# Kernel tuning notes

Measured on AMD Instinct MI355X. Metric: run time of the kernel, lower is better.

The kernel has to match this reference:

```python
import jax, jax.numpy as jnp
import numpy as np

D_IN = 1024
D_OUT = 1024
NUM_HEADS = 16
HEAD_DIM = D_OUT // NUM_HEADS


def setup_inputs() -> dict:
    key = jax.random.key(0)
    ks = jax.random.split(key, 6)
    scale = 0.02
    x = jax.random.normal(ks[0], (8, 1024, D_IN), dtype=jnp.float32)
    # weights stored as [in, out] (transposed vs torch Linear.weight)
    W_query = jax.random.normal(ks[1], (D_IN, D_OUT), dtype=jnp.float32) * scale
    W_key = jax.random.normal(ks[2], (D_IN, HEAD_DIM), dtype=jnp.float32) * scale
    W_value = jax.random.normal(ks[3], (D_IN, HEAD_DIM), dtype=jnp.float32) * scale
    W_out = jax.random.normal(ks[4], (D_OUT, D_OUT), dtype=jnp.float32) * scale
    b_out = jax.random.normal(ks[5], (D_OUT,), dtype=jnp.float32) * scale
    return {"x": x, "W_query": W_query, "W_key": W_key, "W_value": W_value,
            "W_out": W_out, "b_out": b_out}


def reference(x, W_query, W_key, W_value, W_out, b_out):
    B, S, _ = x.shape
    H, Dh = NUM_HEADS, HEAD_DIM
    q = (x @ W_query).reshape(B, S, H, Dh).transpose(0, 2, 1, 3)  # [B,H,S,Dh]
    k = x @ W_key      # [B,S,Dh] single shared head
    v = x @ W_value    # [B,S,Dh]
    # scores: broadcast shared K across all query heads (no explicit repeat)
    scores = jnp.einsum("bhqd,bkd->bhqk", q, k)  # [B,H,S,S]
    causal = jnp.triu(jnp.ones((S, S), dtype=bool), k=1)
    scores = jnp.where(causal[None, None], -jnp.inf, scores)
    attn = jax.nn.softmax(scores / np.sqrt(Dh).astype(np.float32), axis=-1)
    # dropout p=0.0 -> identity
    ctx = jnp.einsum("bhqk,bkd->bhqd", attn, v)  # [B,H,S,Dh]
    ctx = ctx.transpose(0, 2, 1, 3).reshape(B, S, H * Dh)
    return ctx @ W_out + b_out
```

## Files before the change

kernel.cpp:

```cpp
#include <hip/hip_runtime.h>

typedef unsigned short u16;
typedef __attribute__((ext_vector_type(8))) short short8;
typedef __attribute__((ext_vector_type(4))) float f32x4;
typedef __attribute__((ext_vector_type(16))) float f32x16;
typedef __attribute__((ext_vector_type(4))) unsigned short u16x4;
typedef __attribute__((ext_vector_type(4))) int i32x4;

__device__ __forceinline__ u16 f2b(float f) {
  unsigned u = __float_as_uint(f);
  unsigned r = (u + 0x7fffu + ((u >> 16) & 1u)) >> 16;
  return (u16)r;
}

__device__ __forceinline__ void gload16(const u16* g, u16* l) {
  __builtin_amdgcn_global_load_lds((const __attribute__((address_space(1))) void*)g,
                                   (__attribute__((address_space(3))) void*)l, 16, 0, 0);
}

__global__ void cvt_bf16(const float* __restrict__ in, u16* __restrict__ out, int n) {
  int i = (blockIdx.x * blockDim.x + threadIdx.x) * 4;
  if (i >= n) return;
  f32x4 v = *(const f32x4*)(in + i);
  u16x4 o;
  o[0] = f2b(v[0]); o[1] = f2b(v[1]); o[2] = f2b(v[2]); o[3] = f2b(v[3]);
  *(u16x4*)(out + i) = o;
}

__global__ void transpose_cvt(const float* __restrict__ in, u16* __restrict__ out, int R, int C) {
  __shared__ float t[32][33];
  int c0 = blockIdx.x * 32, r0 = blockIdx.y * 32;
  int tx = threadIdx.x & 31, ty = threadIdx.x >> 5;
#pragma unroll
  for (int i = 0; i < 32; i += 8)
    t[ty + i][tx] = in[(size_t)(r0 + ty + i) * C + c0 + tx];
  __syncthreads();
#pragma unroll
  for (int i = 0; i < 32; i += 8)
    out[(size_t)(c0 + ty + i) * R + r0 + tx] = f2b(t[tx][ty + i]);
}

#define GEMM_CORE(A_PTR, B_PTR)                                                        \
  __shared__ u16 As[8192];                                                             \
  __shared__ u16 Bs[8192];                                                             \
  const int tid = threadIdx.x;                                                         \
  const int lane = tid & 63, wid = tid >> 6;                                           \
  const int lg = lane >> 4, li = lane & 15;                                            \
  const int wr = wid >> 1, wc = wid & 1;                                               \
  f32x4 acc[2][4] = {};                                                                \
  const int srow = tid >> 3;                                                \
  const int sslot = tid & 7;                                                           \
  const int scol = 8 * (sslot ^ (srow & 7));              \
  const u16* Ab = (A_PTR) + (size_t)(m0 + srow) * 1024 + scol;                         \
  const u16* Bb = (B_PTR) + (size_t)srow * 1024 + scol;                                \
  u16* AsW = As + wid * 512;                              \
  u16* BsW = Bs + wid * 512;                                                           \
  for (int k0 = 0; k0 < 1024; k0 += 64) {                                              \
    __syncthreads();                                                                   \
    gload16(Ab + k0,         AsW);                                                     \
    gload16(Ab + 65536 + k0, AsW + 4096);                                              \
    gload16(Bb + k0,         BsW);                                                     \
    gload16(Bb + 65536 + k0, BsW + 4096);                                              \
    __syncthreads();                                                                   \
    _Pragma("unroll")                                                                  \
    for (int kki = 0; kki < 2; ++kki) {                                                \
      short8 af[2], bfr[4];                                                            \
      _Pragma("unroll")                                                                \
      for (int mi = 0; mi < 2; ++mi) {                                                 \
        const int r = wr * 32 + mi * 16 + li;                                          \
        af[mi] = *(const short8*)&As[r * 64 + 8 * ((4 * kki + lg) ^ (r & 7))];         \
      }                                                                                \
      _Pragma("unroll")                                                                \
      for (int ni = 0; ni < 4; ++ni) {                                                 \
        const int r = wc * 64 + ni * 16 + li;                                          \
        bfr[ni] = *(const short8*)&Bs[r * 64 + 8 * ((4 * kki + lg) ^ (r & 7))];        \
      }                                                                                \
      _Pragma("unroll")                                                                \
      for (int mi = 0; mi < 2; ++mi)                                                   \
        _Pragma("unroll")                                                              \
        for (int ni = 0; ni < 4; ++ni)                                                 \
          acc[mi][ni] =                                                                \
              __builtin_amdgcn_mfma_f32_16x16x32_bf16(af[mi], bfr[ni], acc[mi][ni],    \
                                                      0, 0, 0);                        \
    }                                                                                  \
  }

__global__ __launch_bounds__(512) void gemm_proj(
    const u16* __restrict__ A, const u16* __restrict__ BtQ, const u16* __restrict__ BtKV,
    u16* __restrict__ Qp, u16* __restrict__ K3, u16* __restrict__ Vt3, float scaleQ) {
  const int m0 = blockIdx.x * 128;
  const int by = blockIdx.y;
  const bool isQ = (by < 8);
  const int n0 = isQ ? by * 128 : 0;
  GEMM_CORE(A, (isQ ? BtQ + (size_t)n0 * 1024 : BtKV))

#pragma unroll
  for (int mi = 0; mi < 2; ++mi) {
#pragma unroll
    for (int ni = 0; ni < 4; ++ni) {
      const int n = n0 + wc * 64 + ni * 16 + li;
#pragma unroll
      for (int i = 0; i < 4; ++i) {
        const int m = m0 + wr * 32 + mi * 16 + lg * 4 + i;
        const float v = acc[mi][ni][i];
        const int bb = m >> 10, ss = m & 1023;
        const int qt = ss >> 5, sl = ss & 31;
        if (isQ) {
          const int h = n >> 6, dd = n & 63;
          const int t = dd >> 4, h2 = (dd >> 3) & 1, j = dd & 7;
          Qp[(((((size_t)bb * 16 + h) * 32 + qt) * 4 + t) * 2 + h2) * 256 + sl * 8 + j] =
              f2b(v * scaleQ);
        } else if (n < 64) {
          const int t = n >> 4, h2 = (n >> 3) & 1, j = n & 7;
          K3[(((((size_t)bb * 32 + qt) * 4 + t) * 2 + h2) * 32 + sl) * 8 + j] = f2b(v);
        } else {
          const int d = n - 64;
          const int ks = sl >> 4, rem = sl & 15;
          const int h2 = (rem >> 2) & 1, j = (rem & 3) | ((rem >> 3) << 2);
          Vt3[(((((size_t)bb * 32 + qt) * 2 + ks) * 2 + h2) * 64 + d) * 8 + j] = f2b(v);
        }
      }
    }
  }
}

__global__ __launch_bounds__(512) void gemm_out(
    const u16* __restrict__ A, const u16* __restrict__ Bt,
    float* __restrict__ Cf, const float* __restrict__ bias) {
  const int m0 = blockIdx.x * 128;
  const int n0 = blockIdx.y * 128;
  GEMM_CORE(A, Bt + (size_t)n0 * 1024)

#pragma unroll
  for (int mi = 0; mi < 2; ++mi)
#pragma unroll
    for (int ni = 0; ni < 4; ++ni) {
      const int n = n0 + wc * 64 + ni * 16 + li;
#pragma unroll
      for (int i = 0; i < 4; ++i) {
        const int m = m0 + wr * 32 + mi * 16 + lg * 4 + i;
        Cf[(size_t)m * 1024 + n] = acc[mi][ni][i] + bias[n];
      }
    }
}

__global__ __launch_bounds__(256, 4) void attn_mqa6(
    const u16* __restrict__ qp, const u16* __restrict__ k3,
    const u16* __restrict__ vt3, u16* __restrict__ paro, float* __restrict__ pl) {
  __shared__ u16 lk[2][2048];
  __shared__ u16 lv[2][2048];
  const int lane = threadIdx.x & 63, wid = threadIdx.x >> 6;
  const int bx = blockIdx.x;
  const int qt = 31 - (bx >> 6);
  const int s  = (bx >> 5) & 1;
  const int g  = bx & 31;
  const int b  = g >> 2;
  const int h  = (g & 3) * 4 + wid;
  const int l31 = lane & 31, hi = lane >> 5;
  const int n0t = (qt + 2) >> 1;
  const int kb_ = s ? n0t : 0;
  const int ke  = s ? qt + 1 : n0t;
  const int task = (b * 16 + h) * 32 + qt;

  const u16* k3b = k3 + (size_t)b * 65536;
  const u16* v3b = vt3 + (size_t)b * 65536;
  const int soff = wid * 512 + lane * 8;

  const u16* qbase = qp + (size_t)task * 2048 + hi * 256 + l31 * 8;
  short8 qa[4];
#pragma unroll
  for (int t = 0; t < 4; ++t) qa[t] = *(const short8*)(qbase + t * 512);

  f32x16 acc0 = {}, acc1 = {};
  float lsum = 0.f;

  if (kb_ < ke) {
    gload16(k3b + (size_t)kb_ * 2048 + soff, &lk[0][wid * 512]);
    gload16(v3b + (size_t)kb_ * 2048 + soff, &lv[0][wid * 512]);
    __syncthreads();

    int par = 0;
    for (int kvt = kb_; kvt < ke; ++kvt, par ^= 1) {
      if (kvt + 1 < ke) {
        gload16(k3b + (size_t)(kvt + 1) * 2048 + soff, &lk[par ^ 1][wid * 512]);
        gload16(v3b + (size_t)(kvt + 1) * 2048 + soff, &lv[par ^ 1][wid * 512]);
      }
      short8 kc[4];
#pragma unroll
      for (int t = 0; t < 4; ++t)
        kc[t] = *(const short8*)&lk[par][l31 * 8 + (t * 2 + hi) * 256];
      const u16* vtt = &lv[par][hi * 512 + l31 * 8];
      const short8 vf0 = *(const short8*)(vtt);
      const short8 vf1 = *(const short8*)(vtt + 1024);
      const short8 vf2 = *(const short8*)(vtt + 256);
      const short8 vf3 = *(const short8*)(vtt + 1280);

      f32x16 st = {};
#pragma unroll
      for (int t = 0; t < 4; ++t)
        st = __builtin_amdgcn_mfma_f32_32x32x16_bf16(kc[t], qa[t], st, 0, 0, 0);

      if (kvt == qt) {
#pragma unroll
        for (int r = 0; r < 16; ++r) {
          const int crow = (r & 3) + 8 * (r >> 2) + 4 * hi;
          if (crow > l31) st[r] = -1e38f;
        }
      }
      float e[16];
#pragma unroll
      for (int r = 0; r < 16; ++r)
        asm("v_exp_f32 %0, %1" : "=v"(e[r]) : "v"(st[r]));
      lsum += ((e[0] + e[1]) + (e[2] + e[3])) + ((e[4] + e[5]) + (e[6] + e[7])) +
              (((e[8] + e[9]) + (e[10] + e[11])) + ((e[12] + e[13]) + (e[14] + e[15])));

      unsigned pw0, pw1, pw2, pw3, pw4, pw5, pw6, pw7;
      asm("v_cvt_pk_bf16_f32 %0, %1, %2" : "=v"(pw0) : "v"(e[0]),  "v"(e[1]));
      asm("v_cvt_pk_bf16_f32 %0, %1, %2" : "=v"(pw1) : "v"(e[2]),  "v"(e[3]));
      asm("v_cvt_pk_bf16_f32 %0, %1, %2" : "=v"(pw2) : "v"(e[4]),  "v"(e[5]));
      asm("v_cvt_pk_bf16_f32 %0, %1, %2" : "=v"(pw3) : "v"(e[6]),  "v"(e[7]));
      asm("v_cvt_pk_bf16_f32 %0, %1, %2" : "=v"(pw4) : "v"(e[8]),  "v"(e[9]));
      asm("v_cvt_pk_bf16_f32 %0, %1, %2" : "=v"(pw5) : "v"(e[10]), "v"(e[11]));
      asm("v_cvt_pk_bf16_f32 %0, %1, %2" : "=v"(pw6) : "v"(e[12]), "v"(e[13]));
      asm("v_cvt_pk_bf16_f32 %0, %1, %2" : "=v"(pw7) : "v"(e[14]), "v"(e[15]));
      i32x4 w0 = {(int)pw0, (int)pw1, (int)pw2, (int)pw3};
      i32x4 w1 = {(int)pw4, (int)pw5, (int)pw6, (int)pw7};
      const short8 pa0 = *(const short8*)&w0;
      const short8 pa1 = *(const short8*)&w1;

      acc0 = __builtin_amdgcn_mfma_f32_32x32x16_bf16(pa0, vf0, acc0, 0, 0, 0);
      acc0 = __builtin_amdgcn_mfma_f32_32x32x16_bf16(pa1, vf1, acc0, 0, 0, 0);
      acc1 = __builtin_amdgcn_mfma_f32_32x32x16_bf16(pa0, vf2, acc1, 0, 0, 0);
      acc1 = __builtin_amdgcn_mfma_f32_32x32x16_bf16(pa1, vf3, acc1, 0, 0, 0);

      __syncthreads();
    }
  }

  const float lfull = lsum + __shfl_xor(lsum, 32, 64);
  u16* pbase = paro + ((size_t)task * 2 + s) * 2048;
#pragma unroll
  for (int r = 0; r < 16; ++r) {
    const int crow = (r & 3) + 8 * (r >> 2) + 4 * hi;
    pbase[crow * 64 + l31] = f2b(acc0[r]);
    pbase[crow * 64 + 32 + l31] = f2b(acc1[r]);
  }
  if (hi == 0) pl[((size_t)task * 2 + s) * 32 + l31] = lfull;
}

__global__ __launch_bounds__(256) void attn_combine(
    const u16* __restrict__ paro, const float* __restrict__ pl, u16* __restrict__ ctxb) {
  const int grp = threadIdx.x >> 6, tid = threadIdx.x & 63;
  const int task = blockIdx.x * 4 + grp;
  const int qt = task & 31, hh = (task >> 5) & 15, bb = task >> 9;
  const unsigned* p0 = (const unsigned*)(paro + (size_t)task * 4096);
  const unsigned* p1 = p0 + 1024;
  const float* lt = pl + (size_t)task * 64;
  const int rh = tid >> 5, cc = tid & 31;
  unsigned* co = (unsigned*)ctxb;
#pragma unroll 4
  for (int it = 0; it < 16; ++it) {
    const int r = it * 2 + rh;
    const float inv = 1.0f / (lt[r] + lt[32 + r]);
    const unsigned a = p0[r * 32 + cc], bu = p1[r * 32 + cc];
    const float v0 = (__uint_as_float(a << 16) + __uint_as_float(bu << 16)) * inv;
    const float v1 = (__uint_as_float(a & 0xffff0000u) + __uint_as_float(bu & 0xffff0000u)) * inv;
    const unsigned pk = (unsigned)f2b(v0) | ((unsigned)f2b(v1) << 16);
    co[(size_t)(bb * 1024 + qt * 32 + r) * 512 + hh * 32 + cc] = pk;
  }
}

extern "C" void kernel_launch(void* const* d_in, const int* in_sizes, int n_in,
                              void* d_out, int out_size, void* d_ws, size_t ws_size,
                              hipStream_t stream) {
  const float* x  = (const float*)d_in[0];
  const float* Wq = (const float*)d_in[1];
  const float* Wk = (const float*)d_in[2];
  const float* Wv = (const float*)d_in[3];
  const float* Wo = (const float*)d_in[4];
  const float* bo = (const float*)d_in[5];
  float* out = (float*)d_out;

  u16* ws16 = (u16*)d_ws;
  const size_t M1 = 1u << 20;
  u16* woT  = ws16;
  u16* qp   = ws16 + 1 * M1;
  u16* k3   = ws16 + 9 * M1;
  u16* vt3  = ws16 + 9 * M1 + (M1 >> 1);
  u16* xb   = ws16 + 10 * M1;
  u16* wqT  = ws16 + 18 * M1;
  u16* wkT  = ws16 + 19 * M1;
  u16* wvT  = wkT + 65536;
  u16* paro = ws16 + 10 * M1;
  float* pl = (float*)(ws16 + 26 * M1);
  u16* ctx  = qp;

  cvt_bf16<<<8192, 256, 0, stream>>>(x, xb, 8192 * 1024);
  transpose_cvt<<<dim3(32, 32), 256, 0, stream>>>(Wq, wqT, 1024, 1024);
  transpose_cvt<<<dim3(2, 32), 256, 0, stream>>>(Wk, wkT, 1024, 64);
  transpose_cvt<<<dim3(2, 32), 256, 0, stream>>>(Wv, wvT, 1024, 64);
  transpose_cvt<<<dim3(32, 32), 256, 0, stream>>>(Wo, woT, 1024, 1024);

  const float SCL = 0.125f * 1.44269504088896340736f;
  gemm_proj<<<dim3(64, 9), 512, 0, stream>>>(xb, wqT, wkT, qp, k3, vt3, SCL);

  attn_mqa6<<<2048, 256, 0, stream>>>(qp, k3, vt3, paro, pl);
  attn_combine<<<1024, 256, 0, stream>>>(paro, pl, ctx);

  gemm_out<<<dim3(64, 8), 512, 0, stream>>>(ctx, woT, out, bo);
}
```

Before: 117.2 us.

## Double-buffer GEMM LDS tiles to overlap global loads with MFMA

Converts the shared GEMM core from a single LDS buffer with two barriers per K-step to a ping-pong pair of buffers. The next K-tile is prefetched via global_load_lds while MFMAs run on the current tile, leaving one barrier per iteration. This doubles LDS use per block (64 KB), which may lower occupancy. Correctness depends on the async LDS loads having completed by the time the barrier is reached.

```diff
diff --git a/kernel.cpp b/kernel.cpp
--- a/kernel.cpp
+++ b/kernel.cpp
@@ -41,8 +41,8 @@
 }
 
 #define GEMM_CORE(A_PTR, B_PTR)                                                        \
-  __shared__ u16 As[8192];                                                             \
-  __shared__ u16 Bs[8192];                                                             \
+  __shared__ u16 As[2][8192];                                                          \
+  __shared__ u16 Bs[2][8192];                                                          \
   const int tid = threadIdx.x;                                                         \
   const int lane = tid & 63, wid = tid >> 6;                                           \
   const int lg = lane >> 4, li = lane & 15;                                            \
@@ -53,27 +53,34 @@
   const int scol = 8 * (sslot ^ (srow & 7));              \
   const u16* Ab = (A_PTR) + (size_t)(m0 + srow) * 1024 + scol;                         \
   const u16* Bb = (B_PTR) + (size_t)srow * 1024 + scol;                                \
-  u16* AsW = As + wid * 512;                              \
-  u16* BsW = Bs + wid * 512;                                                           \
-  for (int k0 = 0; k0 < 1024; k0 += 64) {                                              \
-    __syncthreads();                                                                   \
-    gload16(Ab + k0,         AsW);                                                     \
-    gload16(Ab + 65536 + k0, AsW + 4096);                                              \
-    gload16(Bb + k0,         BsW);                                                     \
-    gload16(Bb + 65536 + k0, BsW + 4096);                                              \
-    __syncthreads();                                                                   \
+  const int wo512 = wid * 512;                             \
+  gload16(Ab,         &As[0][wo512]);                                                  \
+  gload16(Ab + 65536, &As[0][wo512 + 4096]);                                           \
+  gload16(Bb,         &Bs[0][wo512]);                                                  \
+  gload16(Bb + 65536, &Bs[0][wo512 + 4096]);                                           \
+  __syncthreads();                                                                     \
+  _Pragma("unroll 2")                                                                  \
+  for (int t = 0; t < 16; ++t) {                                                       \
+    const int cur = t & 1;                                                             \
+    if (t < 15) {                                     \
+      const int k1 = (t + 1) * 64;                                                     \
+      gload16(Ab + k1,         &As[cur ^ 1][wo512]);                                   \
+      gload16(Ab + 65536 + k1, &As[cur ^ 1][wo512 + 4096]);                            \
+      gload16(Bb + k1,         &Bs[cur ^ 1][wo512]);                                   \
+      gload16(Bb + 65536 + k1, &Bs[cur ^ 1][wo512 + 4096]);                            \
+    }                                                                                  \
     _Pragma("unroll")                                                                  \
     for (int kki = 0; kki < 2; ++kki) {                                                \
       short8 af[2], bfr[4];                                                            \
       _Pragma("unroll")                                                                \
       for (int mi = 0; mi < 2; ++mi) {                                                 \
         const int r = wr * 32 + mi * 16 + li;                                          \
-        af[mi] = *(const short8*)&As[r * 64 + 8 * ((4 * kki + lg) ^ (r & 7))];         \
+        af[mi] = *(const short8*)&As[cur][r * 64 + 8 * ((4 * kki + lg) ^ (r & 7))];    \
       }                                                                                \
       _Pragma("unroll")                                                                \
       for (int ni = 0; ni < 4; ++ni) {                                                 \
         const int r = wc * 64 + ni * 16 + li;                                          \
-        bfr[ni] = *(const short8*)&Bs[r * 64 + 8 * ((4 * kki + lg) ^ (r & 7))];        \
+        bfr[ni] = *(const short8*)&Bs[cur][r * 64 + 8 * ((4 * kki + lg) ^ (r & 7))];   \
       }                                                                                \
       _Pragma("unroll")                                                                \
       for (int mi = 0; mi < 2; ++mi)                                                   \
@@ -83,6 +90,7 @@
               __builtin_amdgcn_mfma_f32_16x16x32_bf16(af[mi], bfr[ni], acc[mi][ni],    \
                                                       0, 0, 0);                        \
     }                                                                                  \
+    __syncthreads();        \
   }
 
 __global__ __launch_bounds__(512) void gemm_proj(
```

Result: no change. 119.3 us (+1.8%).
